# Kernel tuning notes

Measured on AMD Instinct MI355X. Metric: run time of the kernel, lower is better.

The kernel has to match this reference:

```python
import jax, jax.numpy as jnp
import numpy as np

B, T, R, D, E, H, V = 128, 20, 49, 2048, 512, 512, 10000
EPS = 1e-5


def setup_inputs() -> dict:
    key = jax.random.key(0)
    ks = jax.random.split(key, 16)
    f = lambda k, shp: jax.random.normal(k, shp, jnp.float32) * 0.02
    return dict(
        captions=jax.random.randint(ks[0], (B, T), 0, V),
        features=jax.random.normal(ks[1], (B, R, D), jnp.float32),
        emb=f(ks[2], (V, E)),
        Wa=f(ks[3], (H, D)), ba=jnp.zeros((H,), jnp.float32),
        Ua=f(ks[4], (H, H)), bu=jnp.zeros((H,), jnp.float32),
        va=f(ks[5], (1, H)), bv=jnp.zeros((1,), jnp.float32),
        W_ih=f(ks[6], (4 * H, E + D)), b_ih=jnp.zeros((4 * H,), jnp.float32),
        W_hh=f(ks[7], (4 * H, H)), b_hh=jnp.zeros((4 * H,), jnp.float32),
        g1=jnp.ones((H,), jnp.float32), be1=jnp.zeros((H,), jnp.float32),
        fc_w=f(ks[8], (256, H)), fc_b=jnp.zeros((256,), jnp.float32),
        g2=jnp.ones((256,), jnp.float32), be2=jnp.zeros((256,), jnp.float32),
        fc2_w=f(ks[9], (V, 256)), fc2_b=jnp.zeros((V,), jnp.float32),
        ih_w=f(ks[10], (H, D)), ih_b=jnp.zeros((H,), jnp.float32),
        ic_w=f(ks[11], (H, D)), ic_b=jnp.zeros((H,), jnp.float32),
    )


def _bn(x, g, b):
    # BatchNorm1d, training mode: biased batch stats over the batch axis
    m = x.mean(axis=0)
    v = x.var(axis=0)
    return (x - m) * jax.lax.rsqrt(v + EPS) * g + b


def reference(captions, features, emb, Wa, ba, Ua, bu, va, bv,
              W_ih, b_ih, W_hh, b_hh, g1, be1, fc_w, fc_b,
              g2, be2, fc2_w, fc2_b, ih_w, ih_b, ic_w, ic_b):
    embed = emb[captions]                               # [B,T,E]
    mean_f = features.mean(axis=1)                      # [B,D]
    h0 = mean_f @ ih_w.T + ih_b                         # [B,H]
    c0 = mean_f @ ic_w.T + ic_b                         # [B,H]
    # precompute W_a(features): invariant over timesteps
    att1 = jnp.einsum('brd,hd->brh', features, Wa) + ba  # [B,R,H]

    def step(carry, we):
        h, c = carry
        # Bahdanau additive attention
        a2 = h @ Ua.T + bu                              # [B,H]
        score = jnp.tanh(att1 + a2[:, None, :]) @ va[0] + bv[0]   # [B,R]
        w = jax.nn.softmax(score, axis=1)               # [B,R]
        ctx = jnp.einsum('br,brd->bd', w, features)     # [B,D]
        # LSTMCell (torch gate order: i, f, g, o)
        x = jnp.concatenate([we, ctx], axis=1)          # [B,E+D]
        gates = x @ W_ih.T + b_ih + h @ W_hh.T + b_hh   # [B,4H]
        i, fg, g_, o = jnp.split(gates, 4, axis=1)
        i, fg, o = jax.nn.sigmoid(i), jax.nn.sigmoid(fg), jax.nn.sigmoid(o)
        g_ = jnp.tanh(g_)
        c = fg * c + i * g_
        h = o * jnp.tanh(c)
        # NOTE: original reassigns h = B1(h) -> carried state is post-BN
        h = _bn(h, g1, be1)
        out = jax.nn.relu(h @ fc_w.T + fc_b)            # [B,256]
        out = _bn(out, g2, be2)
        out = out @ fc2_w.T + fc2_b                     # [B,V]
        return (h, c), (out, w)

    (_, _), (outs, ws) = jax.lax.scan(step, (h0, c0), embed.transpose(1, 0, 2))
    outputs = outs.transpose(1, 0, 2)                   # [B,T,V]
    atten_weights = ws.transpose(1, 0, 2)               # [B,T,R]
    return outputs, atten_weights
```

## Files before the change

kernel.cpp:

```cpp
#include <hip/hip_runtime.h>
#include <hip/hip_bf16.h>
#include <math.h>

typedef __hip_bfloat16 bf16;
typedef short bf16x8 __attribute__((ext_vector_type(8)));
typedef float f32x4 __attribute__((ext_vector_type(4)));

#define BQ 128
#define TT 20
#define RR 49
#define DD 2048
#define EE 512
#define HH 512
#define VV 10000
#define XW 3072
constexpr float EPSV = 1e-5f;
#define APITCH 40

__device__ __forceinline__ float sigmoidf(float x) { return 1.f / (1.f + __expf(-x)); }
__device__ __forceinline__ float tanh_fast(float x) {
  float e = __expf(2.f * x);
  return 1.f - 2.f / (e + 1.f);
}
__device__ __forceinline__ bf16 f2b(float v) { return __float2bfloat16(v); }
__device__ __forceinline__ float b2f(bf16 v) { return __bfloat162float(v); }

__global__ __launch_bounds__(256) void gemm_mfma(
    const bf16* __restrict__ A, const bf16* __restrict__ W,
    const float* __restrict__ bias,
    float* __restrict__ Cf, bf16* __restrict__ Cb, bf16* __restrict__ Cb2,
    long ldc, long ldc2, int N, int K, int act, int transC) {
  __shared__ __align__(16) short Alds[128 * APITCH];
  __shared__ __align__(16) short Wlds[64 * APITCH];
  int tid = threadIdx.x;
  int bm = blockIdx.y * 128, bn = blockIdx.x * 64;
  int w = tid >> 6, l = tid & 63;
  int lr = l & 15, lq = l >> 4;
  int srow = tid >> 2, skq = (tid & 3) * 8;
  const bf16* pa0 = A + (long)(bm + srow) * K + skq;
  const bf16* pa1 = pa0 + (long)64 * K;
  const bf16* pw = W + (long)(bn + srow) * K + skq;
  bool wok = (bn + srow) < N;
  f32x4 acc[2][4] = {};
  uint4 ra0 = *(const uint4*)pa0;
  uint4 ra1 = *(const uint4*)pa1;
  uint4 rw = wok ? *(const uint4*)pw : make_uint4(0, 0, 0, 0);
  for (int k0 = 0; k0 < K; k0 += 32) {
    __syncthreads();
    *(uint4*)&Alds[srow * APITCH + skq] = ra0;
    *(uint4*)&Alds[(srow + 64) * APITCH + skq] = ra1;
    *(uint4*)&Wlds[srow * APITCH + skq] = rw;
    if (k0 + 32 < K) {
      ra0 = *(const uint4*)(pa0 + k0 + 32);
      ra1 = *(const uint4*)(pa1 + k0 + 32);
      rw = wok ? *(const uint4*)(pw + k0 + 32) : make_uint4(0, 0, 0, 0);
    }
    __syncthreads();
    bf16x8 af[2], bfr[4];
#pragma unroll
    for (int mt = 0; mt < 2; ++mt)
      af[mt] = *(const bf16x8*)&Alds[(w * 32 + mt * 16 + lr) * APITCH + lq * 8];
#pragma unroll
    for (int nt = 0; nt < 4; ++nt)
      bfr[nt] = *(const bf16x8*)&Wlds[(nt * 16 + lr) * APITCH + lq * 8];
#pragma unroll
    for (int mt = 0; mt < 2; ++mt)
#pragma unroll
      for (int nt = 0; nt < 4; ++nt)
        acc[mt][nt] = __builtin_amdgcn_mfma_f32_16x16x32_bf16(
            af[mt], bfr[nt], acc[mt][nt], 0, 0, 0);
  }
#pragma unroll
  for (int mt = 0; mt < 2; ++mt) {
    int gm = bm + w * 32 + mt * 16 + lq * 4;
#pragma unroll
    for (int nt = 0; nt < 4; ++nt) {
      int gn = bn + nt * 16 + lr;
      if (gn >= N) continue;
      float bv = bias ? bias[gn] : 0.f;
#pragma unroll
      for (int i = 0; i < 4; ++i) {
        float v = acc[mt][nt][i] + bv;
        if (act) v = fmaxf(v, 0.f);
        long row = gm + i;
        if (Cf) {
          if (transC) Cf[(long)gn * ldc + row] = v;
          else Cf[row * ldc + gn] = v;
        }
        if (Cb) Cb[row * ldc + gn] = f2b(v);
        if (Cb2) Cb2[row * ldc2 + gn] = f2b(v);
      }
    }
  }
}

__global__ void mean_kernel(const bf16* __restrict__ feat, bf16* __restrict__ meanbf) {
  int idx = blockIdx.x * blockDim.x + threadIdx.x;
  if (idx >= BQ * DD) return;
  int b = idx / DD, d = idx - b * DD;
  const bf16* p = feat + (long)b * RR * DD + d;
  float s = 0.f;
  for (int r = 0; r < RR; ++r) s += b2f(p[(long)r * DD]);
  meanbf[idx] = f2b(s * (1.f / RR));
}

__global__ void f2b_kernel(const float* __restrict__ src, bf16* __restrict__ dst, long n4) {
  long i = (long)blockIdx.x * blockDim.x + threadIdx.x;
  if (i >= n4) return;
  float4 v = ((const float4*)src)[i];
  bf16 o[4] = {f2b(v.x), f2b(v.y), f2b(v.z), f2b(v.w)};
  *(ushort4*)(dst + i * 4) = *(const ushort4*)o;
}

__global__ void wcat_kernel(const float* __restrict__ W_ih, const float* __restrict__ W_hh,
                            bf16* __restrict__ Wcat) {
  int n = blockIdx.y;
  int kc = (blockIdx.x * blockDim.x + threadIdx.x) * 4;
  float4 v = (kc < EE + DD) ? *(const float4*)(W_ih + (long)n * (EE + DD) + kc)
                            : *(const float4*)(W_hh + (long)n * HH + (kc - EE - DD));
  bf16 o[4] = {f2b(v.x), f2b(v.y), f2b(v.z), f2b(v.w)};
  *(ushort4*)(Wcat + (long)n * XW + kc) = *(const ushort4*)o;
}

__global__ void biasc_kernel(const float* __restrict__ b_ih, const float* __restrict__ b_hh,
                             float* __restrict__ bc) {
  int i = blockIdx.x * blockDim.x + threadIdx.x;
  if (i < 4 * HH) bc[i] = b_ih[i] + b_hh[i];
}

__global__ void transpose_ua(const float* __restrict__ Ua, bf16* __restrict__ UaT) {
  __shared__ float tile[64][65];
  int tx = threadIdx.x & 63, ty = threadIdx.x >> 6;
  int c0 = blockIdx.x * 64, k0 = blockIdx.y * 64;
  for (int r = ty; r < 64; r += 4)
    tile[r][tx] = Ua[(long)(c0 + r) * HH + k0 + tx];
  __syncthreads();
  for (int r = ty; r < 64; r += 4)
    UaT[(long)(k0 + r) * HH + c0 + tx] = f2b(tile[tx][r]);
}

__global__ void embed_all_kernel(const int* __restrict__ cap, const float* __restrict__ emb,
                                 bf16* __restrict__ xcat_all) {
  long idx = (long)blockIdx.x * blockDim.x + threadIdx.x;
  int bt = (int)(idx >> 7);
  int e4 = ((int)idx & 127) * 4;
  int b = bt / TT, t = bt - b * TT;
  int tok = cap[b * TT + t];
  float4 v = *(const float4*)(emb + (long)tok * EE + e4);
  bf16 o[4] = {f2b(v.x), f2b(v.y), f2b(v.z), f2b(v.w)};
  *(ushort4*)(xcat_all + ((long)t * BQ + b) * XW + e4) = *(const ushort4*)o;
}

__global__ __launch_bounds__(512) void step_attn_fc(
    const bf16* __restrict__ att1, const bf16* __restrict__ hbf,
    const bf16* __restrict__ UaT, const float* __restrict__ bu,
    const float* __restrict__ va, const float* __restrict__ bv,
    const bf16* __restrict__ feat, bf16* __restrict__ xcat,
    float* __restrict__ att_out, int t, int do_attn,
    const bf16* __restrict__ fcw, const float* __restrict__ fcb,
    const float* __restrict__ g2, const float* __restrict__ be2,
    bf16* __restrict__ out2, int do_fc) {
  __shared__ __align__(16) char smem[29824];
  int blk = blockIdx.x, tid = threadIdx.x;
  if (blk < 128) {
    if (!do_attn) return;
    int b = blk;
    float* hs = (float*)smem;
    float* vas = hs + 512;
    float* a2s = vas + 512;
    float* a2p = a2s + 512;
    float* sc = a2p + 1024;
    hs[tid] = b2f(hbf[b * HH + tid]);
    vas[tid] = va[tid];
    __syncthreads();
    {
      int half = tid >> 8, cp = (tid & 255) * 2;
      const bf16* up = UaT + (long)(half * 256) * HH + cp;
      const float* hh = hs + half * 256;
      float a0 = 0.f, a1 = 0.f;
#pragma unroll 8
      for (int k = 0; k < 256; ++k) {
        uint u = *(const uint*)(up + (long)k * HH);
        float hk = hh[k];
        a0 += hk * b2f(((const bf16*)&u)[0]);
        a1 += hk * b2f(((const bf16*)&u)[1]);
      }
      a2p[half * 512 + cp] = a0;
      a2p[half * 512 + cp + 1] = a1;
    }
    __syncthreads();
    if (tid < 256) {
      int ch = tid * 2;
      a2s[ch] = a2p[ch] + a2p[512 + ch] + bu[ch];
      a2s[ch + 1] = a2p[ch + 1] + a2p[512 + ch + 1] + bu[ch + 1];
    }
    __syncthreads();
    int wave = tid >> 6, lane = tid & 63;
    float vreg[8], areg[8];
    *(float4*)&vreg[0] = *(const float4*)&vas[lane * 8];
    *(float4*)&vreg[4] = *(const float4*)&vas[lane * 8 + 4];
    *(float4*)&areg[0] = *(const float4*)&a2s[lane * 8];
    *(float4*)&areg[4] = *(const float4*)&a2s[lane * 8 + 4];
    for (int r = wave; r < RR; r += 8) {
      bf16 rv[8];
      *(uint4*)rv = *(const uint4*)(att1 + ((long)b * RR + r) * HH + lane * 8);
      float p = 0.f;
#pragma unroll
      for (int j = 0; j < 8; ++j)
        p += vreg[j] * tanh_fast(b2f(rv[j]) + areg[j]);
#pragma unroll
      for (int off = 32; off > 0; off >>= 1) p += __shfl_down(p, off, 64);
      if (lane == 0) sc[r] = p + bv[0];
    }
    __syncthreads();
    if (tid < 64) {
      float v = (tid < RR) ? sc[tid] : -1e30f;
      float m = v;
#pragma unroll
      for (int off = 32; off > 0; off >>= 1) m = fmaxf(m, __shfl_xor(m, off, 64));
      float e = (tid < RR) ? __expf(v - m) : 0.f;
      float s = e;
#pragma unroll
      for (int off = 32; off > 0; off >>= 1) s += __shfl_xor(s, off, 64);
      float wgt = e / s;
      if (tid < RR) {
        sc[tid] = wgt;
        att_out[((long)b * TT + t) * RR + tid] = wgt;
      }
    }
    __syncthreads();
    const bf16* fb = feat + (long)b * RR * DD + tid * 4;
    float ac[4] = {};
    for (int r = 0; r < RR; ++r) {
      uint2 u = *(const uint2*)(fb + (long)r * DD);
      const bf16* pv = (const bf16*)&u;
      float wr = sc[r];
#pragma unroll
      for (int j = 0; j < 4; ++j) ac[j] += wr * b2f(pv[j]);
    }
    bf16 ov[4];
#pragma unroll
    for (int j = 0; j < 4; ++j) ov[j] = f2b(ac[j]);
    *(uint2*)(xcat + (long)b * XW + EE + tid * 4) = *(const uint2*)ov;
  } else {
    if (!do_fc) return;
    int ch0 = (blk - 128) * 8;
    short* wlds = (short*)smem;
    short* hlds = wlds + 4096;
    float* red = (float*)(smem + (4096 + 8704) * 2);
    float* stat = red + 8 * 130;
    const int HP = 68;
    *(bf16x8*)&wlds[tid * 8] = *(const bf16x8*)(fcw + (long)ch0 * HH + tid * 8);
    int b = tid & 127, cg = tid >> 7;
    float acc2[2] = {0.f, 0.f};
    int srow = tid >> 3, sc8 = (tid & 7) * 8;
    for (int k0 = 0; k0 < HH; k0 += 64) {
      __syncthreads();
      *(uint4*)&hlds[srow * HP + sc8] =
          *(const uint4*)(hbf + (long)srow * HH + k0 + sc8);
      *(uint4*)&hlds[(srow + 64) * HP + sc8] =
          *(const uint4*)(hbf + (long)(srow + 64) * HH + k0 + sc8);
      __syncthreads();
#pragma unroll
      for (int kk = 0; kk < 64; kk += 8) {
        bf16 hv[8];
        *(uint4*)hv = *(const uint4*)&hlds[b * HP + kk];
        float hf[8];
#pragma unroll
        for (int j = 0; j < 8; ++j) hf[j] = b2f(hv[j]);
#pragma unroll
        for (int jc = 0; jc < 2; ++jc) {
          const bf16* wr = (const bf16*)&wlds[(cg * 2 + jc) * 512 + k0 + kk];
#pragma unroll
          for (int j = 0; j < 8; ++j) acc2[jc] += hf[j] * b2f(wr[j]);
        }
      }
    }
    float val2[2], dv2[2];
#pragma unroll
    for (int jc = 0; jc < 2; ++jc) {
      int cl = cg * 2 + jc;
      val2[jc] = fmaxf(acc2[jc] + fcb[ch0 + cl], 0.f);
      red[cl * 130 + b] = val2[jc];
    }
    __syncthreads();
    if (tid < 8) {
      float s = 0.f;
      for (int i = 0; i < 128; i += 4)
        s += red[tid * 130 + i] + red[tid * 130 + i + 1] +
             red[tid * 130 + i + 2] + red[tid * 130 + i + 3];
      stat[tid] = s * (1.f / 128);
    }
    __syncthreads();
#pragma unroll
    for (int jc = 0; jc < 2; ++jc) {
      int cl = cg * 2 + jc;
      dv2[jc] = val2[jc] - stat[cl];
      red[cl * 130 + b] = dv2[jc] * dv2[jc];
    }
    __syncthreads();
    if (tid < 8) {
      float s = 0.f;
      for (int i = 0; i < 128; i += 4)
        s += red[tid * 130 + i] + red[tid * 130 + i + 1] +
             red[tid * 130 + i + 2] + red[tid * 130 + i + 3];
      stat[tid] = 1.f / sqrtf(s * (1.f / 128) + EPSV);
    }
    __syncthreads();
#pragma unroll
    for (int jc = 0; jc < 2; ++jc) {
      int cl = cg * 2 + jc;
      out2[(long)b * 256 + ch0 + cl] =
          f2b(dv2[jc] * stat[cl] * g2[ch0 + cl] + be2[ch0 + cl]);
    }
  }
}

__global__ __launch_bounds__(256) void step_gemms(
    const bf16* __restrict__ xc, const bf16* __restrict__ Wcat,
    const float* __restrict__ biasc, float* __restrict__ gatesT,
    const bf16* __restrict__ out2, const bf16* __restrict__ fc2w,
    const float* __restrict__ fc2b, float* __restrict__ outp,
    int do_gates, int do_fc2) {
  __shared__ __align__(16) short Alds[128 * APITCH];
  __shared__ __align__(16) short Wlds[64 * APITCH];
  int blk = blockIdx.x, tid = threadIdx.x;
  int w = tid >> 6, l = tid & 63;
  int lr = l & 15, lq = l >> 4;
  int srow = tid >> 2, skq = (tid & 3) * 8;
  if (blk < 128) {
    if (!do_gates) return;
    const int KC = XW / 4;
    int bn = (blk & 31) * 64, kz = blk >> 5, kbeg = kz * KC;
    const bf16* pa0 = xc + (long)srow * XW + kbeg + skq;
    const bf16* pa1 = pa0 + (long)64 * XW;
    const bf16* pw = Wcat + (long)(bn + srow) * XW + kbeg + skq;
    f32x4 acc[2][4] = {};
    uint4 ra0 = *(const uint4*)pa0;
    uint4 ra1 = *(const uint4*)pa1;
    uint4 rw = *(const uint4*)pw;
    for (int k0 = 0; k0 < KC; k0 += 32) {
      __syncthreads();
      *(uint4*)&Alds[srow * APITCH + skq] = ra0;
      *(uint4*)&Alds[(srow + 64) * APITCH + skq] = ra1;
      *(uint4*)&Wlds[srow * APITCH + skq] = rw;
      if (k0 + 32 < KC) {
        ra0 = *(const uint4*)(pa0 + k0 + 32);
        ra1 = *(const uint4*)(pa1 + k0 + 32);
        rw = *(const uint4*)(pw + k0 + 32);
      }
      __syncthreads();
      bf16x8 af[2], bfr[4];
#pragma unroll
      for (int mt = 0; mt < 2; ++mt)
        af[mt] = *(const bf16x8*)&Alds[(w * 32 + mt * 16 + lr) * APITCH + lq * 8];
#pragma unroll
      for (int nt = 0; nt < 4; ++nt)
        bfr[nt] = *(const bf16x8*)&Wlds[(nt * 16 + lr) * APITCH + lq * 8];
#pragma unroll
      for (int mt = 0; mt < 2; ++mt)
#pragma unroll
        for (int nt = 0; nt < 4; ++nt)
          acc[mt][nt] = __builtin_amdgcn_mfma_f32_16x16x32_bf16(
              af[mt], bfr[nt], acc[mt][nt], 0, 0, 0);
    }
    float* Cf = gatesT + (long)kz * 4 * HH * 128;
#pragma unroll
    for (int mt = 0; mt < 2; ++mt) {
      int gm = w * 32 + mt * 16 + lq * 4;
#pragma unroll
      for (int nt = 0; nt < 4; ++nt) {
        int gn = bn + nt * 16 + lr;
        float bv = (kz == 0) ? biasc[gn] : 0.f;
#pragma unroll
        for (int i = 0; i < 4; ++i)
          Cf[(long)gn * 128 + gm + i] = acc[mt][nt][i] + bv;
      }
    }
  } else {
    if (!do_fc2) return;
    int bn = (blk - 128) * 64;
    const bf16* pa0 = out2 + (long)srow * 256 + skq;
    const bf16* pa1 = pa0 + (long)64 * 256;
    const bf16* pw = fc2w + (long)(bn + srow) * 256 + skq;
    bool wok = (bn + srow) < VV;
    f32x4 acc[2][4] = {};
    uint4 ra0 = *(const uint4*)pa0;
    uint4 ra1 = *(const uint4*)pa1;
    uint4 rw = wok ? *(const uint4*)pw : make_uint4(0, 0, 0, 0);
    for (int k0 = 0; k0 < 256; k0 += 32) {
      __syncthreads();
      *(uint4*)&Alds[srow * APITCH + skq] = ra0;
      *(uint4*)&Alds[(srow + 64) * APITCH + skq] = ra1;
      *(uint4*)&Wlds[srow * APITCH + skq] = rw;
      if (k0 + 32 < 256) {
        ra0 = *(const uint4*)(pa0 + k0 + 32);
        ra1 = *(const uint4*)(pa1 + k0 + 32);
        rw = wok ? *(const uint4*)(pw + k0 + 32) : make_uint4(0, 0, 0, 0);
      }
      __syncthreads();
      bf16x8 af[2], bfr[4];
#pragma unroll
      for (int mt = 0; mt < 2; ++mt)
        af[mt] = *(const bf16x8*)&Alds[(w * 32 + mt * 16 + lr) * APITCH + lq * 8];
#pragma unroll
      for (int nt = 0; nt < 4; ++nt)
        bfr[nt] = *(const bf16x8*)&Wlds[(nt * 16 + lr) * APITCH + lq * 8];
#pragma unroll
      for (int mt = 0; mt < 2; ++mt)
#pragma unroll
        for (int nt = 0; nt < 4; ++nt)
          acc[mt][nt] = __builtin_amdgcn_mfma_f32_16x16x32_bf16(
              af[mt], bfr[nt], acc[mt][nt], 0, 0, 0);
    }
    const long ldc = (long)TT * VV;
#pragma unroll
    for (int mt = 0; mt < 2; ++mt) {
      int gm = w * 32 + mt * 16 + lq * 4;
#pragma unroll
      for (int nt = 0; nt < 4; ++nt) {
        int gn = bn + nt * 16 + lr;
        if (gn >= VV) continue;
        float bv = fc2b[gn];
#pragma unroll
        for (int i = 0; i < 4; ++i)
          outp[(long)(gm + i) * ldc + gn] = acc[mt][nt][i] + bv;
      }
    }
  }
}

__global__ __launch_bounds__(256) void lstm_bn2(
    const float* __restrict__ gatesT, float* __restrict__ cT,
    bf16* __restrict__ hbf, bf16* __restrict__ xnext,
    const float* __restrict__ g1, const float* __restrict__ be1) {
  int tid = threadIdx.x;
  int b = tid & 127, sub = tid >> 7;
  int ch = blockIdx.x * 2 + sub;
  const long GP = (long)4 * HH * 128;
  float vi = 0.f, vf = 0.f, vg = 0.f, vo = 0.f;
#pragma unroll
  for (int z = 0; z < 4; ++z) {
    const float* gz = gatesT + z * GP + (long)ch * 128 + b;
    vi += gz[0 * HH * 128];
    vf += gz[1 * HH * 128];
    vg += gz[2 * HH * 128];
    vo += gz[3 * HH * 128];
  }
  float ig = sigmoidf(vi), fg = sigmoidf(vf), gg = tanh_fast(vg), og = sigmoidf(vo);
  float cn = fg * cT[ch * 128 + b] + ig * gg;
  cT[ch * 128 + b] = cn;
  float hr = og * tanh_fast(cn);
  __shared__ float s1[2][128];
  s1[sub][b] = hr;
  __syncthreads();
  for (int off = 64; off > 0; off >>= 1) {
    if (b < off) s1[sub][b] += s1[sub][b + off];
    __syncthreads();
  }
  float mean = s1[sub][0] * (1.f / 128);
  __syncthreads();
  float dv = hr - mean;
  s1[sub][b] = dv * dv;
  __syncthreads();
  for (int off = 64; off > 0; off >>= 1) {
    if (b < off) s1[sub][b] += s1[sub][b + off];
    __syncthreads();
  }
  float var = s1[sub][0] * (1.f / 128);
  float res = dv * (1.f / sqrtf(var + EPSV)) * g1[ch] + be1[ch];
  hbf[(long)b * HH + ch] = f2b(res);
  xnext[(long)b * XW + EE + DD + ch] = f2b(res);
}

extern "C" void kernel_launch(void* const* d_in, const int* in_sizes, int n_in,
                              void* d_out, int out_size, void* d_ws, size_t ws_size,
                              hipStream_t stream) {
  const int* captions  = (const int*)d_in[0];
  const float* features = (const float*)d_in[1];
  const float* emb   = (const float*)d_in[2];
  const float* Wa    = (const float*)d_in[3];
  const float* ba    = (const float*)d_in[4];
  const float* Ua    = (const float*)d_in[5];
  const float* bu    = (const float*)d_in[6];
  const float* va    = (const float*)d_in[7];
  const float* bv    = (const float*)d_in[8];
  const float* W_ih  = (const float*)d_in[9];
  const float* b_ih  = (const float*)d_in[10];
  const float* W_hh  = (const float*)d_in[11];
  const float* b_hh  = (const float*)d_in[12];
  const float* g1    = (const float*)d_in[13];
  const float* be1   = (const float*)d_in[14];
  const float* fc_w  = (const float*)d_in[15];
  const float* fc_b  = (const float*)d_in[16];
  const float* g2    = (const float*)d_in[17];
  const float* be2   = (const float*)d_in[18];
  const float* fc2_w = (const float*)d_in[19];
  const float* fc2_b = (const float*)d_in[20];
  const float* ih_w  = (const float*)d_in[21];
  const float* ih_b  = (const float*)d_in[22];
  const float* ic_w  = (const float*)d_in[23];
  const float* ic_b  = (const float*)d_in[24];

  float* out = (float*)d_out;
  float* att_out = out + (long)BQ * TT * VV;

  char* p = (char*)d_ws;
  auto alloc = [&](size_t bytes) { char* r = p; p += (bytes + 255) & ~255ULL; return r; };
  bf16* featbf = (bf16*)alloc((size_t)BQ * RR * DD * 2);
  bf16* meanbf = (bf16*)alloc((size_t)BQ * DD * 2);
  bf16* Wcat   = (bf16*)alloc((size_t)4 * HH * XW * 2);
  bf16* Wabf   = (bf16*)alloc((size_t)HH * DD * 2);
  bf16* UaTbf  = (bf16*)alloc((size_t)HH * HH * 2);
  bf16* fcwbf  = (bf16*)alloc((size_t)256 * HH * 2);
  bf16* fc2wbf = (bf16*)alloc((size_t)VV * 256 * 2);
  bf16* ihwbf  = (bf16*)alloc((size_t)HH * DD * 2);
  bf16* icwbf  = (bf16*)alloc((size_t)HH * DD * 2);
  bf16* att1bf = (bf16*)alloc((size_t)BQ * RR * HH * 2);
  bf16* xcat_all = (bf16*)alloc((size_t)(TT + 1) * BQ * XW * 2);
  bf16* hbf    = (bf16*)alloc((size_t)BQ * HH * 2);
  bf16* out2bf = (bf16*)alloc((size_t)BQ * 256 * 2);
  float* biasc = (float*)alloc((size_t)4 * HH * 4);
  float* cT    = (float*)alloc((size_t)BQ * HH * 4);
  float* gatesT = (float*)alloc((size_t)4 * BQ * 4 * HH * 4);

  f2b_kernel<<<(BQ * RR * DD / 4 + 255) / 256, 256, 0, stream>>>(features, featbf, BQ * RR * DD / 4);
  f2b_kernel<<<(HH * DD / 4 + 255) / 256, 256, 0, stream>>>(Wa, Wabf, HH * DD / 4);
  transpose_ua<<<dim3(8, 8), 256, 0, stream>>>(Ua, UaTbf);
  f2b_kernel<<<(256 * HH / 4 + 255) / 256, 256, 0, stream>>>(fc_w, fcwbf, 256 * HH / 4);
  f2b_kernel<<<(VV * 256 / 4 + 255) / 256, 256, 0, stream>>>(fc2_w, fc2wbf, VV * 256 / 4);
  f2b_kernel<<<(HH * DD / 4 + 255) / 256, 256, 0, stream>>>(ih_w, ihwbf, HH * DD / 4);
  f2b_kernel<<<(HH * DD / 4 + 255) / 256, 256, 0, stream>>>(ic_w, icwbf, HH * DD / 4);
  wcat_kernel<<<dim3(XW / 4 / 256, 4 * HH), 256, 0, stream>>>(W_ih, W_hh, Wcat);
  biasc_kernel<<<(4 * HH + 255) / 256, 256, 0, stream>>>(b_ih, b_hh, biasc);
  mean_kernel<<<(BQ * DD + 255) / 256, 256, 0, stream>>>(featbf, meanbf);
  embed_all_kernel<<<(BQ * TT * EE / 4) / 256, 256, 0, stream>>>(captions, emb, xcat_all);

  gemm_mfma<<<dim3(HH / 64, 1), 256, 0, stream>>>(
      meanbf, ihwbf, ih_b, nullptr, hbf, xcat_all + EE + DD, HH, XW, HH, DD, 0, 0);
  gemm_mfma<<<dim3(HH / 64, 1), 256, 0, stream>>>(
      meanbf, icwbf, ic_b, cT, nullptr, nullptr, 128, 0, HH, DD, 0, 1);
  gemm_mfma<<<dim3(HH / 64, BQ * RR / 128), 256, 0, stream>>>(
      featbf, Wabf, ba, nullptr, att1bf, nullptr, HH, 0, HH, DD, 0, 0);

  for (int t = 0; t < TT; ++t) {
    bf16* xc = xcat_all + (size_t)t * BQ * XW;
    bf16* xn = xcat_all + (size_t)(t + 1) * BQ * XW;
    step_attn_fc<<<160, 512, 0, stream>>>(
        att1bf, hbf, UaTbf, bu, va, bv, featbf, xc, att_out, t, 1,
        fcwbf, fc_b, g2, be2, out2bf, t > 0 ? 1 : 0);
    step_gemms<<<285, 256, 0, stream>>>(
        xc, Wcat, biasc, gatesT, out2bf, fc2wbf, fc2_b,
        out + (long)(t > 0 ? t - 1 : 0) * VV, 1, t > 0 ? 1 : 0);
    lstm_bn2<<<HH / 2, 256, 0, stream>>>(gatesT, cT, hbf, xn, g1, be1);
  }
  step_attn_fc<<<160, 512, 0, stream>>>(
      att1bf, hbf, UaTbf, bu, va, bv, featbf, xcat_all, att_out, 0, 0,
      fcwbf, fc_b, g2, be2, out2bf, 1);
  step_gemms<<<285, 256, 0, stream>>>(
      xcat_all, Wcat, biasc, gatesT, out2bf, fc2wbf, fc2_b,
      out + (long)(TT - 1) * VV, 0, 1);
}
```

Measured before the change: 1.474 ms.

## Fuse LSTM cell and BatchNorm into gate GEMM via last-block split-K reduction

```diff
diff --git a/kernel.cpp b/kernel.cpp
--- a/kernel.cpp
+++ b/kernel.cpp
@@ -115,17 +115,22 @@
 __global__ void wcat_kernel(const float* __restrict__ W_ih, const float* __restrict__ W_hh,
                             bf16* __restrict__ Wcat) {
   int n = blockIdx.y;
+  int src = (n & 3) * HH + (n >> 2);
   int kc = (blockIdx.x * blockDim.x + threadIdx.x) * 4;
-  float4 v = (kc < EE + DD) ? *(const float4*)(W_ih + (long)n * (EE + DD) + kc)
-                            : *(const float4*)(W_hh + (long)n * HH + (kc - EE - DD));
+  float4 v = (kc < EE + DD) ? *(const float4*)(W_ih + (long)src * (EE + DD) + kc)
+                            : *(const float4*)(W_hh + (long)src * HH + (kc - EE - DD));
   bf16 o[4] = {f2b(v.x), f2b(v.y), f2b(v.z), f2b(v.w)};
   *(ushort4*)(Wcat + (long)n * XW + kc) = *(const ushort4*)o;
 }
 
 __global__ void biasc_kernel(const float* __restrict__ b_ih, const float* __restrict__ b_hh,
-                             float* __restrict__ bc) {
+                             float* __restrict__ bc, int* __restrict__ cnt) {
   int i = blockIdx.x * blockDim.x + threadIdx.x;
-  if (i < 4 * HH) bc[i] = b_ih[i] + b_hh[i];
+  if (i < 4 * HH) {
+    int src = (i & 3) * HH + (i >> 2);
+    bc[i] = b_ih[src] + b_hh[src];
+  }
+  if (i < TT * 32) cnt[i] = 0;
 }
 
 __global__ void transpose_ua(const float* __restrict__ Ua, bf16* __restrict__ UaT) {
@@ -321,9 +326,13 @@
     const float* __restrict__ biasc, float* __restrict__ gatesT,
     const bf16* __restrict__ out2, const bf16* __restrict__ fc2w,
     const float* __restrict__ fc2b, float* __restrict__ outp,
-    int do_gates, int do_fc2) {
+    int* __restrict__ cnt, float* __restrict__ cT,
+    bf16* __restrict__ hbf, bf16* __restrict__ xnext,
+    const float* __restrict__ g1, const float* __restrict__ be1,
+    int t, int do_gates, int do_fc2) {
   __shared__ __align__(16) short Alds[128 * APITCH];
   __shared__ __align__(16) short Wlds[64 * APITCH];
+  __shared__ int lastflag;
   int blk = blockIdx.x, tid = threadIdx.x;
   int w = tid >> 6, l = tid & 63;
   int lr = l & 15, lq = l >> 4;
@@ -331,7 +340,8 @@
   if (blk < 128) {
     if (!do_gates) return;
     const int KC = XW / 4;
-    int bn = (blk & 31) * 64, kz = blk >> 5, kbeg = kz * KC;
+    int tile = blk & 31, kz = blk >> 5;
+    int bn = tile * 64, kbeg = kz * KC;
     const bf16* pa0 = xc + (long)srow * XW + kbeg + skq;
     const bf16* pa1 = pa0 + (long)64 * XW;
     const bf16* pw = Wcat + (long)(bn + srow) * XW + kbeg + skq;
@@ -364,7 +374,8 @@
           acc[mt][nt] = __builtin_amdgcn_mfma_f32_16x16x32_bf16(
               af[mt], bfr[nt], acc[mt][nt], 0, 0, 0);
     }
-    float* Cf = gatesT + (long)kz * 4 * HH * 128;
+    const long GP = (long)4 * HH * 128;
+    float* Cf = gatesT + (long)kz * GP;
 #pragma unroll
     for (int mt = 0; mt < 2; ++mt) {
       int gm = w * 32 + mt * 16 + lq * 4;
@@ -376,6 +387,83 @@
         for (int i = 0; i < 4; ++i)
           Cf[(long)gn * 128 + gm + i] = acc[mt][nt][i] + bv;
       }
+    }
+    __threadfence();
+    __syncthreads();
+    if (tid == 0) lastflag = (atomicAdd(&cnt[t * 32 + tile], 1) == 3);
+    __syncthreads();
+    if (!lastflag) return;
+    __threadfence();
+    int ch_l = tid >> 4, b0 = (tid & 15) * 8;
+    int ch = (bn >> 2) + ch_l;
+    float gv[4][8];
+#pragma unroll
+    for (int g = 0; g < 4; ++g) {
+      int gn = bn + ch_l * 4 + g;
+      const float* s0 = gatesT + (long)gn * 128 + b0;
+      float4 x0 = *(const float4*)s0;
+      float4 x1 = *(const float4*)(s0 + 4);
+#pragma unroll
+      for (int z = 1; z < 4; ++z) {
+        const float* sz = s0 + z * GP;
+        float4 y0 = *(const float4*)sz;
+        float4 y1 = *(const float4*)(sz + 4);
+        x0.x += y0.x; x0.y += y0.y; x0.z += y0.z; x0.w += y0.w;
+        x1.x += y1.x; x1.y += y1.y; x1.z += y1.z; x1.w += y1.w;
+      }
+      gv[g][0] = x0.x; gv[g][1] = x0.y; gv[g][2] = x0.z; gv[g][3] = x0.w;
+      gv[g][4] = x1.x; gv[g][5] = x1.y; gv[g][6] = x1.z; gv[g][7] = x1.w;
+    }
+    float* cp = cT + (long)ch * 128 + b0;
+    float4 c0v = *(const float4*)cp;
+    float4 c1v = *(const float4*)(cp + 4);
+    float cold[8] = {c0v.x, c0v.y, c0v.z, c0v.w, c1v.x, c1v.y, c1v.z, c1v.w};
+    float hr[8];
+#pragma unroll
+    for (int i = 0; i < 8; ++i) {
+      float ig = sigmoidf(gv[0][i]);
+      float fg = sigmoidf(gv[1][i]);
+      float gg = tanh_fast(gv[2][i]);
+      float og = sigmoidf(gv[3][i]);
+      float cn = fg * cold[i] + ig * gg;
+      cold[i] = cn;
+      hr[i] = og * tanh_fast(cn);
+    }
+    *(float4*)cp = make_float4(cold[0], cold[1], cold[2], cold[3]);
+    *(float4*)(cp + 4) = make_float4(cold[4], cold[5], cold[6], cold[7]);
+    float* red = (float*)Alds;
+    int bgrp = tid & 15;
+    float s = 0.f;
+#pragma unroll
+    for (int i = 0; i < 8; ++i) s += hr[i];
+    red[ch_l * 17 + bgrp] = s;
+    __syncthreads();
+    __shared__ float mstat[16], vstat[16];
+    if (tid < 16) {
+      float m = 0.f;
+      for (int j = 0; j < 16; ++j) m += red[tid * 17 + j];
+      mstat[tid] = m * (1.f / 128);
+    }
+    __syncthreads();
+    float mean = mstat[ch_l];
+    float dv[8];
+    float sv = 0.f;
+#pragma unroll
+    for (int i = 0; i < 8; ++i) { dv[i] = hr[i] - mean; sv += dv[i] * dv[i]; }
+    red[ch_l * 17 + bgrp] = sv;
+    __syncthreads();
+    if (tid < 16) {
+      float m = 0.f;
+      for (int j = 0; j < 16; ++j) m += red[tid * 17 + j];
+      vstat[tid] = 1.f / sqrtf(m * (1.f / 128) + EPSV);
+    }
+    __syncthreads();
+    float rstd = vstat[ch_l], gg1 = g1[ch], bb1 = be1[ch];
+#pragma unroll
+    for (int i = 0; i < 8; ++i) {
+      bf16 res = f2b(dv[i] * rstd * gg1 + bb1);
+      hbf[(long)(b0 + i) * HH + ch] = res;
+      xnext[(long)(b0 + i) * XW + EE + DD + ch] = res;
     }
   } else {
     if (!do_fc2) return;
@@ -428,49 +516,6 @@
       }
     }
   }
-}
-
-__global__ __launch_bounds__(256) void lstm_bn2(
-    const float* __restrict__ gatesT, float* __restrict__ cT,
-    bf16* __restrict__ hbf, bf16* __restrict__ xnext,
-    const float* __restrict__ g1, const float* __restrict__ be1) {
-  int tid = threadIdx.x;
-  int b = tid & 127, sub = tid >> 7;
-  int ch = blockIdx.x * 2 + sub;
-  const long GP = (long)4 * HH * 128;
-  float vi = 0.f, vf = 0.f, vg = 0.f, vo = 0.f;
-#pragma unroll
-  for (int z = 0; z < 4; ++z) {
-    const float* gz = gatesT + z * GP + (long)ch * 128 + b;
-    vi += gz[0 * HH * 128];
-    vf += gz[1 * HH * 128];
-    vg += gz[2 * HH * 128];
-    vo += gz[3 * HH * 128];
-  }
-  float ig = sigmoidf(vi), fg = sigmoidf(vf), gg = tanh_fast(vg), og = sigmoidf(vo);
-  float cn = fg * cT[ch * 128 + b] + ig * gg;
-  cT[ch * 128 + b] = cn;
-  float hr = og * tanh_fast(cn);
-  __shared__ float s1[2][128];
-  s1[sub][b] = hr;
-  __syncthreads();
-  for (int off = 64; off > 0; off >>= 1) {
-    if (b < off) s1[sub][b] += s1[sub][b + off];
-    __syncthreads();
-  }
-  float mean = s1[sub][0] * (1.f / 128);
-  __syncthreads();
-  float dv = hr - mean;
-  s1[sub][b] = dv * dv;
-  __syncthreads();
-  for (int off = 64; off > 0; off >>= 1) {
-    if (b < off) s1[sub][b] += s1[sub][b + off];
-    __syncthreads();
-  }
-  float var = s1[sub][0] * (1.f / 128);
-  float res = dv * (1.f / sqrtf(var + EPSV)) * g1[ch] + be1[ch];
-  hbf[(long)b * HH + ch] = f2b(res);
-  xnext[(long)b * XW + EE + DD + ch] = f2b(res);
 }
 
 extern "C" void kernel_launch(void* const* d_in, const int* in_sizes, int n_in,
@@ -523,6 +568,7 @@
   float* biasc = (float*)alloc((size_t)4 * HH * 4);
   float* cT    = (float*)alloc((size_t)BQ * HH * 4);
   float* gatesT = (float*)alloc((size_t)4 * BQ * 4 * HH * 4);
+  int* cnt     = (int*)alloc((size_t)TT * 32 * 4);
 
   f2b_kernel<<<(BQ * RR * DD / 4 + 255) / 256, 256, 0, stream>>>(features, featbf, BQ * RR * DD / 4);
   f2b_kernel<<<(HH * DD / 4 + 255) / 256, 256, 0, stream>>>(Wa, Wabf, HH * DD / 4);
@@ -532,7 +578,7 @@
   f2b_kernel<<<(HH * DD / 4 + 255) / 256, 256, 0, stream>>>(ih_w, ihwbf, HH * DD / 4);
   f2b_kernel<<<(HH * DD / 4 + 255) / 256, 256, 0, stream>>>(ic_w, icwbf, HH * DD / 4);
   wcat_kernel<<<dim3(XW / 4 / 256, 4 * HH), 256, 0, stream>>>(W_ih, W_hh, Wcat);
-  biasc_kernel<<<(4 * HH + 255) / 256, 256, 0, stream>>>(b_ih, b_hh, biasc);
+  biasc_kernel<<<(4 * HH + 255) / 256, 256, 0, stream>>>(b_ih, b_hh, biasc, cnt);
   mean_kernel<<<(BQ * DD + 255) / 256, 256, 0, stream>>>(featbf, meanbf);
   embed_all_kernel<<<(BQ * TT * EE / 4) / 256, 256, 0, stream>>>(captions, emb, xcat_all);
 
@@ -551,13 +597,14 @@
         fcwbf, fc_b, g2, be2, out2bf, t > 0 ? 1 : 0);
     step_gemms<<<285, 256, 0, stream>>>(
         xc, Wcat, biasc, gatesT, out2bf, fc2wbf, fc2_b,
-        out + (long)(t > 0 ? t - 1 : 0) * VV, 1, t > 0 ? 1 : 0);
-    lstm_bn2<<<HH / 2, 256, 0, stream>>>(gatesT, cT, hbf, xn, g1, be1);
+        out + (long)(t > 0 ? t - 1 : 0) * VV,
+        cnt, cT, hbf, xn, g1, be1, t, 1, t > 0 ? 1 : 0);
   }
   step_attn_fc<<<160, 512, 0, stream>>>(
       att1bf, hbf, UaTbf, bu, va, bv, featbf, xcat_all, att_out, 0, 0,
       fcwbf, fc_b, g2, be2, out2bf, 1);
   step_gemms<<<285, 256, 0, stream>>>(
       xcat_all, Wcat, biasc, gatesT, out2bf, fc2wbf, fc2_b,
-      out + (long)(TT - 1) * VV, 0, 1);
-}
+      out + (long)(TT - 1) * VV,
+      cnt, cT, hbf, xcat_all, g1, be1, 0, 0, 1);
+}
```

New measurement: 1.810 ms. +22.8%, slower.
